# Performance work log

Measured on AMD Instinct MI355X. Metric: run time of the kernel, lower is better.

Reference implementation:

```python
import jax, jax.numpy as jnp
import numpy as np

NUM_HEADS = 8
LN_EPS = 1e-5


def setup_inputs() -> dict:
    key = jax.random.key(0)
    ks = jax.random.split(key, 12)
    B, L, D = 8, 1000, 512
    dk = D // NUM_HEADS
    max_len = 1000
    s = 1.0 / np.sqrt(D)
    return {
        "x": jax.random.normal(ks[0], (B, L, D), dtype=jnp.float32),
        "Wq": jax.random.normal(ks[1], (D, D), dtype=jnp.float32) * s,
        "bq": jnp.zeros((D,), jnp.float32),
        "Wk": jax.random.normal(ks[2], (D, D), dtype=jnp.float32) * s,
        "bk": jnp.zeros((D,), jnp.float32),
        "Wv": jax.random.normal(ks[3], (D, D), dtype=jnp.float32) * s,
        "bv": jnp.zeros((D,), jnp.float32),
        "Wo": jax.random.normal(ks[4], (D, D), dtype=jnp.float32) * s,
        "bo": jnp.zeros((D,), jnp.float32),
        "rel_pos_embed": jax.random.normal(ks[5], (2 * max_len - 1, dk), dtype=jnp.float32) * 0.05,
        "ln_gamma": jnp.ones((D,), jnp.float32),
        "ln_beta": jnp.zeros((D,), jnp.float32),
    }


def reference(x, Wq, bq, Wk, bk, Wv, bv, Wo, bo, rel_pos_embed, ln_gamma, ln_beta):
    B, L, D = x.shape
    H = NUM_HEADS
    dk = D // H
    residual = x
    # LayerNorm (pre-norm)
    mu = jnp.mean(x, axis=-1, keepdims=True)
    var = jnp.mean(jnp.square(x - mu), axis=-1, keepdims=True)
    xn = (x - mu) * jax.lax.rsqrt(var + LN_EPS) * ln_gamma + ln_beta
    # projections (torch Linear: x @ W.T + b), split heads -> (B, H, L, dk)
    q = (xn @ Wq.T + bq).reshape(B, L, H, dk).transpose(0, 2, 1, 3)
    k = (xn @ Wk.T + bk).reshape(B, L, H, dk).transpose(0, 2, 1, 3)
    v = (xn @ Wv.T + bv).reshape(B, L, H, dk).transpose(0, 2, 1, 3)
    scores = jnp.einsum("bhid,bhjd->bhij", q, k) / jnp.sqrt(jnp.float32(dk))
    # relative position bias: idx[i, j] = j - i + L - 1
    rng = jnp.arange(L)
    rel_idx = rng[None, :] - rng[:, None] + (L - 1)  # (L, L)
    rel = rel_pos_embed[rel_idx]  # (L, L, dk)
    pos_scores = jnp.einsum("bhid,ijd->bhij", q, rel)
    attn = jax.nn.softmax(scores + pos_scores, axis=-1)  # dropout = identity (eval)
    ctx = jnp.einsum("bhij,bhjd->bhid", attn, v)
    ctx = ctx.transpose(0, 2, 1, 3).reshape(B, L, D)
    out = ctx @ Wo.T + bo
    return out + residual
```

## Files before the change

### kernel.cpp

```cpp
#include <hip/hip_runtime.h>
#include <hip/hip_bf16.h>

#define NHEAD 8
#define DK 64
#define DMODEL 512
#define LSEQ 1000
#define TI 64
#define TJ 64
#define NJT 16

typedef __attribute__((ext_vector_type(8))) short bf16x8;
typedef __attribute__((ext_vector_type(4))) float f32x4;

__device__ inline short f2bf(float f) {
    __hip_bfloat16 h = __float2bfloat16(f);
    return *reinterpret_cast<short*>(&h);
}
__device__ inline float bf2f(short s) {
    unsigned int u = ((unsigned int)(unsigned short)s) << 16;
    return __uint_as_float(u);
}
__device__ inline void gload_lds16(const void* g, void* l) {
    __builtin_amdgcn_global_load_lds(
        (const __attribute__((address_space(1))) unsigned int*)g,
        (__attribute__((address_space(3))) unsigned int*)l, 16, 0, 0);
}

__global__ __launch_bounds__(256) void convert_kernel(
    const float* __restrict__ Wq, const float* __restrict__ Wk, const float* __restrict__ Wv,
    const float* __restrict__ Wo, const float* __restrict__ E,
    short* __restrict__ Wqkv_bf, short* __restrict__ Wo_bf, short* __restrict__ E_bf)
{
    int qd = blockIdx.x * 256 + threadIdx.x;
    if (qd < 196608) {
        int flat = qd * 4;
        int row = flat >> 9, col = flat & 511;
        int proj = row >> 9, rrow = row & 511;
        const float* src = proj == 0 ? Wq : (proj == 1 ? Wk : Wv);
        float sc = proj == 0 ? 0.125f : 1.0f;
        float4 x = *(const float4*)&src[(size_t)rrow * 512 + col];
        short t[4] = { f2bf(x.x * sc), f2bf(x.y * sc), f2bf(x.z * sc), f2bf(x.w * sc) };
        *(uint2*)&Wqkv_bf[flat] = *(uint2*)t;
    } else if (qd < 262144) {
        int flat = (qd - 196608) * 4;
        float4 x = *(const float4*)&Wo[flat];
        short t[4] = { f2bf(x.x), f2bf(x.y), f2bf(x.z), f2bf(x.w) };
        *(uint2*)&Wo_bf[flat] = *(uint2*)t;
    } else if (qd < 294128) {
        int flat = (qd - 262144) * 4;
        float4 x = *(const float4*)&E[flat];
        short t[4] = { f2bf(x.x * 8.f), f2bf(x.y * 8.f), f2bf(x.z * 8.f), f2bf(x.w * 8.f) };
        *(uint2*)&E_bf[flat] = *(uint2*)t;
    }
}

__global__ __launch_bounds__(256) void ln_kernel(
    const float* __restrict__ x, const float* __restrict__ gamma,
    const float* __restrict__ beta, short* __restrict__ xn)
{
    int row = blockIdx.x;
    int tid = threadIdx.x;
    const float2* xr = (const float2*)(x + (size_t)row * DMODEL);
    float2 v = xr[tid];
    float s  = v.x + v.y;
    float ss = v.x * v.x + v.y * v.y;
#pragma unroll
    for (int o = 32; o > 0; o >>= 1) {
        s  += __shfl_down(s, o, 64);
        ss += __shfl_down(ss, o, 64);
    }
    __shared__ float red[8];
    int wid = tid >> 6;
    if ((tid & 63) == 0) { red[wid * 2] = s; red[wid * 2 + 1] = ss; }
    __syncthreads();
    s  = red[0] + red[2] + red[4] + red[6];
    ss = red[1] + red[3] + red[5] + red[7];
    float mu  = s * (1.0f / (float)DMODEL);
    float var = ss * (1.0f / (float)DMODEL) - mu * mu;
    float inv = rsqrtf(var + 1e-5f);
    float2 g  = ((const float2*)gamma)[tid];
    float2 bb = ((const float2*)beta)[tid];
    short o2[2];
    o2[0] = f2bf((v.x - mu) * inv * g.x + bb.x);
    o2[1] = f2bf((v.y - mu) * inv * g.y + bb.y);
    *(unsigned int*)&xn[(size_t)row * DMODEL + tid * 2] = *(unsigned int*)o2;
}

template<int MODE>
__global__ __launch_bounds__(256) void gemm_bf16(
    const short* __restrict__ A, const short* __restrict__ W,
    const float* __restrict__ b0, const float* __restrict__ b1, const float* __restrict__ b2,
    short* __restrict__ Oq, short* __restrict__ Ok, short* __restrict__ Ov,
    float* __restrict__ Of, const float* __restrict__ resid)
{
    __shared__ short As[128 * 32];
    __shared__ short Bs[128 * 32];
    const int K = 512;
    const int tid = threadIdx.x;
    const int lane = tid & 63, w = tid >> 6;
    const int m0 = blockIdx.y * 128, n0 = blockIdx.x * 128;
    const int wr = w >> 1, wc = w & 1;

    const int srow = (lane >> 2);
    const int scol = (lane & 3) * 8;
    int ga0 = m0 + (w * 2 + 0) * 16 + srow; if (ga0 > 7999) ga0 = 7999;
    int ga1 = m0 + (w * 2 + 1) * 16 + srow; if (ga1 > 7999) ga1 = 7999;
    const int gb0 = n0 + (w * 2 + 0) * 16 + srow;
    const int gb1 = n0 + (w * 2 + 1) * 16 + srow;

    f32x4 acc[4][4];
#pragma unroll
    for (int i = 0; i < 4; ++i)
#pragma unroll
        for (int j = 0; j < 4; ++j) acc[i][j] = (f32x4){0.f, 0.f, 0.f, 0.f};

    for (int k0 = 0; k0 < K; k0 += 32) {
        __syncthreads();
        gload_lds16(&A[(size_t)ga0 * K + k0 + scol], &As[(w * 2 + 0) * 512]);
        gload_lds16(&A[(size_t)ga1 * K + k0 + scol], &As[(w * 2 + 1) * 512]);
        gload_lds16(&W[(size_t)gb0 * K + k0 + scol], &Bs[(w * 2 + 0) * 512]);
        gload_lds16(&W[(size_t)gb1 * K + k0 + scol], &Bs[(w * 2 + 1) * 512]);
        __syncthreads();

        bf16x8 af[4], bf[4];
#pragma unroll
        for (int fi = 0; fi < 4; ++fi)
            af[fi] = *(bf16x8*)&As[(wr * 64 + fi * 16 + (lane & 15)) * 32 + (lane >> 4) * 8];
#pragma unroll
        for (int fj = 0; fj < 4; ++fj)
            bf[fj] = *(bf16x8*)&Bs[(wc * 64 + fj * 16 + (lane & 15)) * 32 + (lane >> 4) * 8];
#pragma unroll
        for (int fi = 0; fi < 4; ++fi)
#pragma unroll
            for (int fj = 0; fj < 4; ++fj)
                acc[fi][fj] = __builtin_amdgcn_mfma_f32_16x16x32_bf16(af[fi], bf[fj], acc[fi][fj], 0, 0, 0);
    }

#pragma unroll
    for (int fi = 0; fi < 4; ++fi) {
#pragma unroll
        for (int fj = 0; fj < 4; ++fj) {
#pragma unroll
            for (int r = 0; r < 4; ++r) {
                int m = m0 + wr * 64 + fi * 16 + (lane >> 4) * 4 + r;
                if (m >= 8000) continue;
                int n = n0 + wc * 64 + fj * 16 + (lane & 15);
                float val = acc[fi][fj][r];
                if (MODE == 0) {
                    int proj = n >> 9, rem = n & 511;
                    int h = rem >> 6, d = rem & 63;
                    float bias = proj == 0 ? b0[rem] * 0.125f : (proj == 1 ? b1[rem] : b2[rem]);
                    short* O = proj == 0 ? Oq : (proj == 1 ? Ok : Ov);
                    int bb = m / 1000, ii = m - bb * 1000;
                    O[((size_t)(bb * NHEAD + h) * LSEQ + ii) * DK + d] = f2bf(val + bias);
                } else {
                    Of[(size_t)m * DMODEL + n] = val + b0[n] + resid[(size_t)m * DMODEL + n];
                }
            }
        }
    }
}

__global__ __launch_bounds__(256, 2) void attn_mfma(
    const short* __restrict__ q, const short* __restrict__ k,
    const short* __restrict__ v, const short* __restrict__ E,
    short* __restrict__ ctx)
{
    __shared__ short Qs[TI][72];
    __shared__ short Kt[TJ][72];
    __shared__ short Et[128][72];
    __shared__ short Vt[DK][72];
    __shared__ short Pp[TI][136];
    __shared__ short Pl[TI][72];

    const int it = blockIdx.x, h = blockIdx.y, b = blockIdx.z;
    const int i0 = it * TI;
    const int tid = threadIdx.x;
    const int lane = tid & 63, w = tid >> 6;
    const int g = lane >> 4, c = lane & 15;

    const size_t base = (size_t)(b * NHEAD + h) * LSEQ * DK;

#pragma unroll
    for (int rep = 0; rep < 2; ++rep) {
        int id = tid + rep * 256;
        int row = id >> 3, c0 = (id & 7) * 8;
        int gr = i0 + row; if (gr > LSEQ - 1) gr = LSEQ - 1;
        *(int4*)&Qs[row][c0] = *(const int4*)&q[base + (size_t)gr * DK + c0];
    }
    __syncthreads();

    bf16x8 Aq0 = *(bf16x8*)&Qs[w * 16 + c][g * 8];
    bf16x8 Aq1 = *(bf16x8*)&Qs[w * 16 + c][32 + g * 8];

    float mrow[4], lrow[4];
    f32x4 acc[4];
#pragma unroll
    for (int r = 0; r < 4; ++r) { mrow[r] = -1e30f; lrow[r] = 0.f; }
#pragma unroll
    for (int fd = 0; fd < 4; ++fd) acc[fd] = (f32x4){0.f, 0.f, 0.f, 0.f};

    for (int jt = 0; jt < NJT; ++jt) {
        const int j0 = jt * TJ;
        const int d0 = j0 - i0 + (LSEQ - 1) - 63;
        __syncthreads();

#pragma unroll
        for (int rep = 0; rep < 2; ++rep) {
            int id = tid + rep * 256;
            int row = id >> 3, c0 = (id & 7) * 8;
            int gr = j0 + row; if (gr > LSEQ - 1) gr = LSEQ - 1;
            *(int4*)&Kt[row][c0] = *(const int4*)&k[base + (size_t)gr * DK + c0];
        }
#pragma unroll
        for (int rep = 0; rep < 4; ++rep) {
            int id = tid + rep * 256;
            int row = id >> 3, c0 = (id & 7) * 8;
            int dd = d0 + row;
            if (dd < 0) dd = 0;
            if (dd > 2 * LSEQ - 2) dd = 2 * LSEQ - 2;
            *(int4*)&Et[row][c0] = *(const int4*)&E[(size_t)dd * DK + c0];
        }
#pragma unroll
        for (int rep = 0; rep < 4; ++rep) {
            int id = tid + rep * 256;
            int j = id >> 4, dq = (id & 15) * 4;
            int gr = j0 + j; if (gr > LSEQ - 1) gr = LSEQ - 1;
            short t[4];
            *(int2*)t = *(const int2*)&v[base + (size_t)gr * DK + dq];
            Vt[dq + 0][j] = t[0];
            Vt[dq + 1][j] = t[1];
            Vt[dq + 2][j] = t[2];
            Vt[dq + 3][j] = t[3];
        }
        __syncthreads();

#pragma unroll
        for (int fd = 0; fd < 8; ++fd) {
            f32x4 pa = (f32x4){0.f, 0.f, 0.f, 0.f};
            bf16x8 e0 = *(bf16x8*)&Et[fd * 16 + c][g * 8];
            bf16x8 e1 = *(bf16x8*)&Et[fd * 16 + c][32 + g * 8];
            pa = __builtin_amdgcn_mfma_f32_16x16x32_bf16(Aq0, e0, pa, 0, 0, 0);
            pa = __builtin_amdgcn_mfma_f32_16x16x32_bf16(Aq1, e1, pa, 0, 0, 0);
#pragma unroll
            for (int r = 0; r < 4; ++r)
                Pp[w * 16 + g * 4 + r][fd * 16 + c] = f2bf(pa[r]);
        }

        f32x4 sf[4];
#pragma unroll
        for (int fj = 0; fj < 4; ++fj) {
            f32x4 s4 = (f32x4){0.f, 0.f, 0.f, 0.f};
            bf16x8 k0v = *(bf16x8*)&Kt[fj * 16 + c][g * 8];
            bf16x8 k1v = *(bf16x8*)&Kt[fj * 16 + c][32 + g * 8];
            s4 = __builtin_amdgcn_mfma_f32_16x16x32_bf16(Aq0, k0v, s4, 0, 0, 0);
            s4 = __builtin_amdgcn_mfma_f32_16x16x32_bf16(Aq1, k1v, s4, 0, 0, 0);
            sf[fj] = s4;
        }

        float sv[4][4], pm[4];
#pragma unroll
        for (int r = 0; r < 4; ++r) pm[r] = -1e30f;
#pragma unroll
        for (int fj = 0; fj < 4; ++fj) {
            int jl = fj * 16 + c;
            bool valid = (j0 + jl) < LSEQ;
#pragma unroll
            for (int r = 0; r < 4; ++r) {
                int ilt = w * 16 + g * 4 + r;
                int d = jl - ilt + 63;
                float x = sf[fj][r] + bf2f(Pp[ilt][d]);
                if (!valid) x = -1e30f;
                sv[fj][r] = x;
                pm[r] = fmaxf(pm[r], x);
            }
        }
#pragma unroll
        for (int r = 0; r < 4; ++r) {
            float vv = pm[r];
            vv = fmaxf(vv, __shfl_xor(vv, 1));
            vv = fmaxf(vv, __shfl_xor(vv, 2));
            vv = fmaxf(vv, __shfl_xor(vv, 4));
            vv = fmaxf(vv, __shfl_xor(vv, 8));
            pm[r] = vv;
        }
        float psum[4];
#pragma unroll
        for (int r = 0; r < 4; ++r) {
            float mn = fmaxf(mrow[r], pm[r]);
            float sc = __expf(mrow[r] - mn);
            mrow[r] = mn;
            lrow[r] *= sc;
#pragma unroll
            for (int fd = 0; fd < 4; ++fd) acc[fd][r] *= sc;
            psum[r] = 0.f;
        }
#pragma unroll
        for (int fj = 0; fj < 4; ++fj) {
            int jl = fj * 16 + c;
#pragma unroll
            for (int r = 0; r < 4; ++r) {
                float p = __expf(sv[fj][r] - mrow[r]);
                psum[r] += p;
                Pl[w * 16 + g * 4 + r][jl] = f2bf(p);
            }
        }
#pragma unroll
        for (int r = 0; r < 4; ++r) {
            float vv = psum[r];
            vv += __shfl_xor(vv, 1);
            vv += __shfl_xor(vv, 2);
            vv += __shfl_xor(vv, 4);
            vv += __shfl_xor(vv, 8);
            lrow[r] += vv;
        }

#pragma unroll
        for (int ks = 0; ks < 2; ++ks) {
            bf16x8 ap = *(bf16x8*)&Pl[w * 16 + c][ks * 32 + g * 8];
#pragma unroll
            for (int fd = 0; fd < 4; ++fd) {
                bf16x8 bv2 = *(bf16x8*)&Vt[fd * 16 + c][ks * 32 + g * 8];
                acc[fd] = __builtin_amdgcn_mfma_f32_16x16x32_bf16(ap, bv2, acc[fd], 0, 0, 0);
            }
        }
    }

#pragma unroll
    for (int r = 0; r < 4; ++r) {
        int ig = i0 + w * 16 + g * 4 + r;
        if (ig < LSEQ) {
            float inv = 1.0f / lrow[r];
#pragma unroll
            for (int fd = 0; fd < 4; ++fd)
                ctx[((size_t)(b * LSEQ + ig)) * DMODEL + h * DK + fd * 16 + c] =
                    f2bf(acc[fd][r] * inv);
        }
    }
}

extern "C" void kernel_launch(void* const* d_in, const int* in_sizes, int n_in,
                              void* d_out, int out_size, void* d_ws, size_t ws_size,
                              hipStream_t stream)
{
    const float* x     = (const float*)d_in[0];
    const float* Wq    = (const float*)d_in[1];
    const float* bq    = (const float*)d_in[2];
    const float* Wk    = (const float*)d_in[3];
    const float* bk    = (const float*)d_in[4];
    const float* Wv    = (const float*)d_in[5];
    const float* bv    = (const float*)d_in[6];
    const float* Wo    = (const float*)d_in[7];
    const float* bo    = (const float*)d_in[8];
    const float* E     = (const float*)d_in[9];
    const float* gamma = (const float*)d_in[10];
    const float* beta  = (const float*)d_in[11];
    float* out = (float*)d_out;

    const size_t nTok = 8 * LSEQ;
    const size_t nBLD = nTok * DMODEL;
    short* xn_bf   = (short*)d_ws;
    short* qb      = xn_bf + nBLD;
    short* kb      = qb + nBLD;
    short* vb      = kb + nBLD;
    short* ctx_bf  = vb + nBLD;
    short* Wqkv_bf = ctx_bf + nBLD;
    short* Wo_bf   = Wqkv_bf + 1536 * 512;
    short* E_bf    = Wo_bf + 512 * 512;

    convert_kernel<<<1149, 256, 0, stream>>>(Wq, Wk, Wv, Wo, E, Wqkv_bf, Wo_bf, E_bf);
    ln_kernel<<<(int)nTok, 256, 0, stream>>>(x, gamma, beta, xn_bf);
    gemm_bf16<0><<<dim3(12, 63), 256, 0, stream>>>(
        xn_bf, Wqkv_bf, bq, bk, bv, qb, kb, vb, nullptr, nullptr);
    attn_mfma<<<dim3((LSEQ + TI - 1) / TI, NHEAD, 8), 256, 0, stream>>>(
        qb, kb, vb, E_bf, ctx_bf);
    gemm_bf16<1><<<dim3(4, 63), 256, 0, stream>>>(
        ctx_bf, Wo_bf, bo, nullptr, nullptr, nullptr, nullptr, nullptr, out, x);
}
```

Measured before the change: 286.7 us.

## Load rel-pos embeddings into registers, alias Q/P LDS, raise occupancy

The relative-position embedding tile is no longer staged through shared memory. Each lane loads its MFMA operand fragments straight from global memory into registers. The Q tile buffer is reused for the P probabilities, and the V transpose index mapping is changed to reduce LDS bank conflicts. Together these cut LDS usage so the launch bound can go to 3 blocks per CU. The cost is more VGPRs for the 16 embedding fragments and uncoalesced global loads that may spill or stall.

```diff
diff --git a/kernel.cpp b/kernel.cpp
--- a/kernel.cpp
+++ b/kernel.cpp
@@ -161,17 +161,15 @@
     }
 }
 
-__global__ __launch_bounds__(256, 2) void attn_mfma(
+__global__ __launch_bounds__(256, 3) void attn_mfma(
     const short* __restrict__ q, const short* __restrict__ k,
     const short* __restrict__ v, const short* __restrict__ E,
     short* __restrict__ ctx)
 {
-    __shared__ short Qs[TI][72];
+    __shared__ short QsPl[TI][72];
     __shared__ short Kt[TJ][72];
-    __shared__ short Et[128][72];
     __shared__ short Vt[DK][72];
     __shared__ short Pp[TI][136];
-    __shared__ short Pl[TI][72];
 
     const int it = blockIdx.x, h = blockIdx.y, b = blockIdx.z;
     const int i0 = it * TI;
@@ -186,12 +184,12 @@
         int id = tid + rep * 256;
         int row = id >> 3, c0 = (id & 7) * 8;
         int gr = i0 + row; if (gr > LSEQ - 1) gr = LSEQ - 1;
-        *(int4*)&Qs[row][c0] = *(const int4*)&q[base + (size_t)gr * DK + c0];
+        *(int4*)&QsPl[row][c0] = *(const int4*)&q[base + (size_t)gr * DK + c0];
     }
     __syncthreads();
 
-    bf16x8 Aq0 = *(bf16x8*)&Qs[w * 16 + c][g * 8];
-    bf16x8 Aq1 = *(bf16x8*)&Qs[w * 16 + c][32 + g * 8];
+    bf16x8 Aq0 = *(bf16x8*)&QsPl[w * 16 + c][g * 8];
+    bf16x8 Aq1 = *(bf16x8*)&QsPl[w * 16 + c][32 + g * 8];
 
     float mrow[4], lrow[4];
     f32x4 acc[4];
@@ -215,16 +213,8 @@
 #pragma unroll
         for (int rep = 0; rep < 4; ++rep) {
             int id = tid + rep * 256;
-            int row = id >> 3, c0 = (id & 7) * 8;
-            int dd = d0 + row;
-            if (dd < 0) dd = 0;
-            if (dd > 2 * LSEQ - 2) dd = 2 * LSEQ - 2;
-            *(int4*)&Et[row][c0] = *(const int4*)&E[(size_t)dd * DK + c0];
-        }
-#pragma unroll
-        for (int rep = 0; rep < 4; ++rep) {
-            int id = tid + rep * 256;
-            int j = id >> 4, dq = (id & 15) * 4;
+            int j = ((id >> 8) << 4) | (id & 15);
+            int dq = ((id >> 4) & 15) * 4;
             int gr = j0 + j; if (gr > LSEQ - 1) gr = LSEQ - 1;
             short t[4];
             *(int2*)t = *(const int2*)&v[base + (size_t)gr * DK + dq];
@@ -233,15 +223,23 @@
             Vt[dq + 2][j] = t[2];
             Vt[dq + 3][j] = t[3];
         }
+        bf16x8 ef[8][2];
+#pragma unroll
+        for (int fd = 0; fd < 8; ++fd) {
+            int dd = d0 + fd * 16 + c;
+            if (dd < 0) dd = 0;
+            if (dd > 2 * LSEQ - 2) dd = 2 * LSEQ - 2;
+            const short* erow = E + (size_t)dd * DK;
+            ef[fd][0] = *(const bf16x8*)&erow[g * 8];
+            ef[fd][1] = *(const bf16x8*)&erow[32 + g * 8];
+        }
         __syncthreads();
 
 #pragma unroll
         for (int fd = 0; fd < 8; ++fd) {
             f32x4 pa = (f32x4){0.f, 0.f, 0.f, 0.f};
-            bf16x8 e0 = *(bf16x8*)&Et[fd * 16 + c][g * 8];
-            bf16x8 e1 = *(bf16x8*)&Et[fd * 16 + c][32 + g * 8];
-            pa = __builtin_amdgcn_mfma_f32_16x16x32_bf16(Aq0, e0, pa, 0, 0, 0);
-            pa = __builtin_amdgcn_mfma_f32_16x16x32_bf16(Aq1, e1, pa, 0, 0, 0);
+            pa = __builtin_amdgcn_mfma_f32_16x16x32_bf16(Aq0, ef[fd][0], pa, 0, 0, 0);
+            pa = __builtin_amdgcn_mfma_f32_16x16x32_bf16(Aq1, ef[fd][1], pa, 0, 0, 0);
 #pragma unroll
             for (int r = 0; r < 4; ++r)
                 Pp[w * 16 + g * 4 + r][fd * 16 + c] = f2bf(pa[r]);
@@ -302,7 +300,7 @@
             for (int r = 0; r < 4; ++r) {
                 float p = __expf(sv[fj][r] - mrow[r]);
                 psum[r] += p;
-                Pl[w * 16 + g * 4 + r][jl] = f2bf(p);
+                QsPl[w * 16 + g * 4 + r][jl] = f2bf(p);
             }
         }
 #pragma unroll
@@ -317,7 +315,7 @@
 
 #pragma unroll
         for (int ks = 0; ks < 2; ++ks) {
-            bf16x8 ap = *(bf16x8*)&Pl[w * 16 + c][ks * 32 + g * 8];
+            bf16x8 ap = *(bf16x8*)&QsPl[w * 16 + c][ks * 32 + g * 8];
 #pragma unroll
             for (int fd = 0; fd < 4; ++fd) {
                 bf16x8 bv2 = *(bf16x8*)&Vt[fd * 16 + c][ks * 32 + g * 8];
```

After: 350.4 us. 22.2% more time.
